# Kernel optimization log

Hardware: AMD Instinct MI355X
Metric: run time of the kernel (lower is better)

The kernel has to match this reference:

```python
import jax, jax.numpy as jnp
import numpy as np

B, T, C, H = 1, 4096, 512, 8
HS = C // H  # head size = 64
ROPE_BASE = 10000.0


def setup_inputs() -> dict:
    key = jax.random.key(0)
    k1, k2, k3 = jax.random.split(key, 3)
    x = jax.random.normal(k1, (B, T, C), dtype=jnp.float32)
    W_attn = jax.random.normal(k2, (3 * C, C), dtype=jnp.float32) * 0.02
    W_proj = jax.random.normal(k3, (C, C), dtype=jnp.float32) * 0.02
    # RoPE cache: (T, HS//2, 2) = (cos, sin) per position/frequency
    pos = jnp.arange(T, dtype=jnp.float32)
    inv_freq = 1.0 / (ROPE_BASE ** (jnp.arange(0, HS, 2, dtype=jnp.float32) / HS))
    ang = pos[:, None] * inv_freq[None, :]  # (T, HS//2)
    rope = jnp.stack([jnp.cos(ang), jnp.sin(ang)], axis=-1)
    # causal mask (1,1,T,T), True = attend
    mask = jnp.tril(jnp.ones((T, T), dtype=bool))[None, None]
    return {"x": x, "rope": rope, "mask": mask, "W_attn": W_attn, "W_proj": W_proj}


def apply_rope(x, rope):
    # x: (B, T, H, hs); rope: (>=T, hs//2, 2)
    b, t, h, d = x.shape
    xs = x.reshape(b, t, h, d // 2, 2)
    rc = rope[:t].reshape(1, t, 1, d // 2, 2)
    real = xs[..., 0] * rc[..., 0] - xs[..., 1] * rc[..., 1]
    imag = xs[..., 1] * rc[..., 0] + xs[..., 0] * rc[..., 1]
    return jnp.stack([real, imag], axis=-1).reshape(b, t, h, d)


def reference(x, rope, mask, W_attn, W_proj):
    b, t, c = x.shape
    qkv = x @ W_attn.T  # (B,T,3C)
    q, k, v = jnp.split(qkv, 3, axis=2)
    q = q.reshape(b, t, H, HS)
    k = k.reshape(b, t, H, HS)
    v = v.reshape(b, t, H, HS)
    q = apply_rope(q, rope)
    k = apply_rope(k, rope)
    # (B,H,T,hs)
    q = q.transpose(0, 2, 1, 3)
    k = k.transpose(0, 2, 1, 3)
    v = v.transpose(0, 2, 1, 3)
    scores = jnp.einsum('bhqd,bhkd->bhqk', q, k) * (1.0 / np.sqrt(HS).astype(np.float32))
    scores = jnp.where(mask, scores, -jnp.inf)
    att = jax.nn.softmax(scores, axis=-1)
    y = jnp.einsum('bhqk,bhkd->bhqd', att, v)
    y = y.transpose(0, 2, 1, 3).reshape(b, t, c)
    return y @ W_proj.T
```

## Files before the change

### kernel.cpp

```cpp
#include <hip/hip_runtime.h>

#define T_ 4096
#define C_ 512
#define H_ 8
#define HS_ 64

typedef __attribute__((ext_vector_type(8))) short s16x8;
typedef __attribute__((ext_vector_type(4))) float f32x4;
typedef unsigned int u32;

__device__ __forceinline__ float bf2f(short u) {
    union { float f; unsigned int i; } v;
    v.i = ((unsigned int)(unsigned short)u) << 16;
    return v.f;
}
__device__ __forceinline__ short f2bf(float f) {
    union { float f; unsigned int i; } v;
    v.f = f;
    unsigned int r = (v.i + 0x7FFFu + ((v.i >> 16) & 1u)) >> 16;
    return (short)r;
}

__device__ __forceinline__ void gload_lds16(const short* g, short* l) {
    __builtin_amdgcn_global_load_lds((const __attribute__((address_space(1))) u32*)g,
                                     (__attribute__((address_space(3))) u32*)l,
                                     16, 0, 0);
}

__global__ void cvt3_kernel(const float* __restrict__ x, const float* __restrict__ wa,
                            const float* __restrict__ wp,
                            short* __restrict__ xb, short* __restrict__ wab,
                            short* __restrict__ wpb) {
    int b = blockIdx.x, tid = threadIdx.x;
    const float* src; short* dst; int i;
    if (b < 2048)      { src = x;  dst = xb;  i = b * 256 + tid; }
    else if (b < 2816) { src = wa; dst = wab; i = (b - 2048) * 256 + tid; }
    else               { src = wp; dst = wpb; i = (b - 2816) * 256 + tid; }
    float4 v = ((const float4*)src)[i];
    short4 o;
    o.x = f2bf(v.x); o.y = f2bf(v.y); o.z = f2bf(v.z); o.w = f2bf(v.w);
    ((short4*)dst)[i] = o;
}

template <int BM, int BN, int OUT_BF16>
__global__ __launch_bounds__(256) void gemm_bt(const short* __restrict__ A,
                                               const short* __restrict__ B,
                                               void* __restrict__ Cv,
                                               int M, int N, int K) {
    __shared__ __align__(16) short As[BM][64];
    __shared__ __align__(16) short Bs[BN][64];
    constexpr int WM = BM / 2, WN = BN / 2;
    constexpr int MR = WM / 16, NR = WN / 16;
    int bn = blockIdx.x, bm = blockIdx.y;
    int tid = threadIdx.x;
    int lane = tid & 63, w = tid >> 6;
    int wr = w >> 1, wc = w & 1;
    int lr = lane & 15, lg = lane >> 4;

    f32x4 acc[MR][NR];
#pragma unroll
    for (int m = 0; m < MR; ++m)
#pragma unroll
        for (int n = 0; n < NR; ++n) acc[m][n] = f32x4{0.f, 0.f, 0.f, 0.f};

    const short* Ab = A + (size_t)bm * BM * K;
    const short* Bb = B + (size_t)bn * BN * K;

    for (int k0 = 0; k0 < K; k0 += 64) {
#pragma unroll
        for (int i = 0; i < BM / 32; ++i) {
            int c = i * 256 + tid;
            int row = c >> 3, cb = (c & 7) ^ (row & 7);
            gload_lds16(Ab + (size_t)row * K + k0 + cb * 8, &As[0][0] + c * 8);
        }
#pragma unroll
        for (int i = 0; i < BN / 32; ++i) {
            int c = i * 256 + tid;
            int row = c >> 3, cb = (c & 7) ^ (row & 7);
            gload_lds16(Bb + (size_t)row * K + k0 + cb * 8, &Bs[0][0] + c * 8);
        }
        __syncthreads();
#pragma unroll
        for (int kk = 0; kk < 2; ++kk) {
            s16x8 af[MR], bf[NR];
#pragma unroll
            for (int m = 0; m < MR; ++m) {
                int row = wr * WM + m * 16 + lr;
                af[m] = *(const s16x8*)&As[row][(((kk * 4 + lg) ^ (row & 7)) << 3)];
            }
#pragma unroll
            for (int n = 0; n < NR; ++n) {
                int row = wc * WN + n * 16 + lr;
                bf[n] = *(const s16x8*)&Bs[row][(((kk * 4 + lg) ^ (row & 7)) << 3)];
            }
#pragma unroll
            for (int m = 0; m < MR; ++m)
#pragma unroll
                for (int n = 0; n < NR; ++n)
                    acc[m][n] = __builtin_amdgcn_mfma_f32_16x16x32_bf16(af[m], bf[n], acc[m][n], 0, 0, 0);
        }
        __syncthreads();
    }

#pragma unroll
    for (int m = 0; m < MR; ++m) {
        int row = bm * BM + wr * WM + m * 16 + lg * 4;
#pragma unroll
        for (int n = 0; n < NR; ++n) {
            int col = bn * BN + wc * WN + n * 16 + lr;
#pragma unroll
            for (int i = 0; i < 4; ++i) {
                size_t idx = (size_t)(row + i) * N + col;
                if (OUT_BF16) ((short*)Cv)[idx] = f2bf(acc[m][n][i]);
                else          ((float*)Cv)[idx] = acc[m][n][i];
            }
        }
    }
}

__global__ __launch_bounds__(256) void prep_kernel(const short* __restrict__ qkv,
                                                   const float* __restrict__ rope,
                                                   short* __restrict__ q,
                                                   short* __restrict__ k,
                                                   short* __restrict__ vt) {
    __shared__ short tile[64][72];
    int bt = blockIdx.x, h = blockIdx.y;
    int tid = threadIdx.x;
    const float QS = 0.18033688011112042f;

#pragma unroll
    for (int r = 0; r < 2; ++r) {
        int idx = r * 256 + tid;
        int tt = idx >> 3, c8 = idx & 7;
        int t = bt * 64 + tt;
        const short* row = qkv + (size_t)t * (3 * C_) + h * 64 + c8 * 8;
        s16x8 qv = *(const s16x8*)row;
        s16x8 kv = *(const s16x8*)(row + C_);
        float4 rc0 = *(const float4*)(rope + t * 64 + c8 * 8);
        float4 rc1 = *(const float4*)(rope + t * 64 + c8 * 8 + 4);
        float cs[4] = {rc0.x, rc0.z, rc1.x, rc1.z};
        float sn[4] = {rc0.y, rc0.w, rc1.y, rc1.w};
        s16x8 qo, ko;
#pragma unroll
        for (int p = 0; p < 4; ++p) {
            float qe = bf2f(qv[2 * p]), qd = bf2f(qv[2 * p + 1]);
            float ke = bf2f(kv[2 * p]), kd = bf2f(kv[2 * p + 1]);
            qo[2 * p]     = f2bf((qe * cs[p] - qd * sn[p]) * QS);
            qo[2 * p + 1] = f2bf((qd * cs[p] + qe * sn[p]) * QS);
            ko[2 * p]     = f2bf(ke * cs[p] - kd * sn[p]);
            ko[2 * p + 1] = f2bf(kd * cs[p] + ke * sn[p]);
        }
        size_t o = ((size_t)h * T_ + t) * HS_ + c8 * 8;
        *(s16x8*)(q + o) = qo;
        *(s16x8*)(k + o) = ko;
    }

#pragma unroll
    for (int it = 0; it < 16; ++it) {
        int idx = it * 256 + tid;
        int dd = idx & 63, tt = idx >> 6;
        tile[tt][dd] = qkv[(size_t)(bt * 64 + tt) * (3 * C_) + 2 * C_ + h * 64 + dd];
    }
    __syncthreads();
#pragma unroll
    for (int it = 0; it < 16; ++it) {
        int idx = it * 256 + tid;
        int tt = idx & 63, dd = idx >> 6;
        vt[((size_t)h * HS_ + dd) * T_ + bt * 64 + tt] = tile[tt][dd];
    }
}

__global__ __launch_bounds__(256) void attn_kernel(const short* __restrict__ q,
                                                   const short* __restrict__ k,
                                                   const short* __restrict__ vt,
                                                   short* __restrict__ ypart,
                                                   float* __restrict__ lpart) {
    __shared__ __align__(16) short Ks[2][64][64];
    __shared__ __align__(16) short Vs[2][64][64];
    __shared__ __align__(16) short P[4][16][64];
    int bx = blockIdx.x;
    int h = bx & 7;
    int u = bx >> 3;
    int qb = 0, j = u;
    for (int qq = 31; qq >= 0; --qq) {
        int ncq = (qq + 4) >> 2;
        if (j < ncq) { qb = qq; break; }
        j -= ncq;
    }
    int ncq = (qb + 4) >> 2;
    int tiles = 2 * qb + 2;
    int bas = tiles / ncq, rr = tiles % ncq;
    int t0 = j * bas + (j < rr ? j : rr);
    int t1 = t0 + bas + (j < rr ? 1 : 0);

    int tid = threadIdx.x;
    int w = tid >> 6, lane = tid & 63;
    int lr = lane & 15, lg = lane >> 4, x7 = lane & 7;
    int qrow0 = qb * 128 + w * 32;
    const float MC = 12.0f;

    const short* qp = q + ((size_t)h * T_ + qrow0 + lr) * HS_ + lg * 8;
    s16x8 aq0 = *(const s16x8*)qp;
    s16x8 aq1 = *(const s16x8*)(qp + 32);
    s16x8 aq2 = *(const s16x8*)(qp + 16 * HS_);
    s16x8 aq3 = *(const s16x8*)(qp + 16 * HS_ + 32);

    s16x8 bones;
#pragma unroll
    for (int jj = 0; jj < 8; ++jj) bones[jj] = (short)0x3F80;

    f32x4 yA[4], yB[4];
#pragma unroll
    for (int n = 0; n < 4; ++n) { yA[n] = f32x4{0.f,0.f,0.f,0.f}; yB[n] = f32x4{0.f,0.f,0.f,0.f}; }
    f32x4 lAa = f32x4{0.f,0.f,0.f,0.f}, lBa = f32x4{0.f,0.f,0.f,0.f};

    const short* kH = k + (size_t)h * T_ * HS_;
    const short* vH = vt + (size_t)h * HS_ * T_;

    auto stage = [&](short* Kb, short* Vb, int t) {
#pragma unroll
        for (int r = 0; r < 2; ++r) {
            int c = r * 256 + tid;
            int row = c >> 3;
            int cb = (c & 7) ^ (row & 7);
            gload_lds16(kH + (size_t)(t * 64 + row) * HS_ + cb * 8, Kb + c * 8);
            gload_lds16(vH + (size_t)row * T_ + t * 64 + cb * 8, Vb + c * 8);
        }
    };

    short* Pw = &P[w][0][0];

    auto body = [&](int t, const short* Kb, const short* Vb) {
        f32x4 sA[4], sB[4];
#pragma unroll
        for (int c4 = 0; c4 < 4; ++c4) {
            int krow = c4 * 16 + lr;
            const short* kp = Kb + krow * 64;
            s16x8 k0 = *(const s16x8*)(kp + ((lg ^ x7) << 3));
            s16x8 k1 = *(const s16x8*)(kp + (((lg + 4) ^ x7) << 3));
            f32x4 s = f32x4{0.f,0.f,0.f,0.f};
            s = __builtin_amdgcn_mfma_f32_16x16x32_bf16(aq0, k0, s, 0, 0, 0);
            sA[c4] = __builtin_amdgcn_mfma_f32_16x16x32_bf16(aq1, k1, s, 0, 0, 0);
            f32x4 s2 = f32x4{0.f,0.f,0.f,0.f};
            s2 = __builtin_amdgcn_mfma_f32_16x16x32_bf16(aq2, k0, s2, 0, 0, 0);
            sB[c4] = __builtin_amdgcn_mfma_f32_16x16x32_bf16(aq3, k1, s2, 0, 0, 0);
        }
        if (t * 64 + 63 > qrow0) {
#pragma unroll
            for (int c4 = 0; c4 < 4; ++c4) {
                int kcol = t * 64 + c4 * 16 + lr;
#pragma unroll
                for (int i = 0; i < 4; ++i)
                    if (kcol > qrow0 + lg * 4 + i) sA[c4][i] = -1e30f;
            }
        }
        if (t * 64 + 63 > qrow0 + 16) {
#pragma unroll
            for (int c4 = 0; c4 < 4; ++c4) {
                int kcol = t * 64 + c4 * 16 + lr;
#pragma unroll
                for (int i = 0; i < 4; ++i)
                    if (kcol > qrow0 + 16 + lg * 4 + i) sB[c4][i] = -1e30f;
            }
        }
        s16x8 vf[8];
#pragma unroll
        for (int n = 0; n < 4; ++n) {
            int vrow = n * 16 + lr;
            const short* vrp = Vb + vrow * 64;
            vf[2 * n]     = *(const s16x8*)(vrp + ((lg ^ (vrow & 7)) << 3));
            vf[2 * n + 1] = *(const s16x8*)(vrp + (((lg + 4) ^ (vrow & 7)) << 3));
        }
#pragma unroll
        for (int c4 = 0; c4 < 4; ++c4)
#pragma unroll
            for (int i = 0; i < 4; ++i) {
                int row = lg * 4 + i;
                int off = row * 64 + (((c4 * 2 + (lr >> 3)) ^ (row & 7)) << 3) + (lr & 7);
                Pw[off] = f2bf(exp2f(sA[c4][i] - MC));
            }
        s16x8 ap0 = *(const s16x8*)&Pw[lr * 64 + ((lg ^ x7) << 3)];
        s16x8 ap1 = *(const s16x8*)&Pw[lr * 64 + (((lg + 4) ^ x7) << 3)];
        lAa = __builtin_amdgcn_mfma_f32_16x16x32_bf16(ap0, bones, lAa, 0, 0, 0);
        lAa = __builtin_amdgcn_mfma_f32_16x16x32_bf16(ap1, bones, lAa, 0, 0, 0);
#pragma unroll
        for (int n = 0; n < 4; ++n) {
            yA[n] = __builtin_amdgcn_mfma_f32_16x16x32_bf16(ap0, vf[2 * n], yA[n], 0, 0, 0);
            yA[n] = __builtin_amdgcn_mfma_f32_16x16x32_bf16(ap1, vf[2 * n + 1], yA[n], 0, 0, 0);
        }
#pragma unroll
        for (int c4 = 0; c4 < 4; ++c4)
#pragma unroll
            for (int i = 0; i < 4; ++i) {
                int row = lg * 4 + i;
                int off = row * 64 + (((c4 * 2 + (lr >> 3)) ^ (row & 7)) << 3) + (lr & 7);
                Pw[off] = f2bf(exp2f(sB[c4][i] - MC));
            }
        s16x8 bp0 = *(const s16x8*)&Pw[lr * 64 + ((lg ^ x7) << 3)];
        s16x8 bp1 = *(const s16x8*)&Pw[lr * 64 + (((lg + 4) ^ x7) << 3)];
        lBa = __builtin_amdgcn_mfma_f32_16x16x32_bf16(bp0, bones, lBa, 0, 0, 0);
        lBa = __builtin_amdgcn_mfma_f32_16x16x32_bf16(bp1, bones, lBa, 0, 0, 0);
#pragma unroll
        for (int n = 0; n < 4; ++n) {
            yB[n] = __builtin_amdgcn_mfma_f32_16x16x32_bf16(bp0, vf[2 * n], yB[n], 0, 0, 0);
            yB[n] = __builtin_amdgcn_mfma_f32_16x16x32_bf16(bp1, vf[2 * n + 1], yB[n], 0, 0, 0);
        }
    };

    stage(&Ks[0][0][0], &Vs[0][0][0], t0);
    __syncthreads();
    int t = t0;
    for (;;) {
        bool m1 = (t + 1 < t1);
        if (m1) stage(&Ks[1][0][0], &Vs[1][0][0], t + 1);
        body(t, &Ks[0][0][0], &Vs[0][0][0]);
        __syncthreads();
        ++t;
        if (!m1) break;
        bool m2 = (t + 1 < t1);
        if (m2) stage(&Ks[0][0][0], &Vs[0][0][0], t + 1);
        body(t, &Ks[1][0][0], &Vs[1][0][0]);
        __syncthreads();
        ++t;
        if (!m2) break;
    }

    short* yp = ypart + (((size_t)j * H_ + h) * T_ + qrow0) * HS_;
#pragma unroll
    for (int n = 0; n < 4; ++n)
#pragma unroll
        for (int i = 0; i < 4; ++i) {
            yp[(size_t)(lg * 4 + i) * HS_ + n * 16 + lr]      = f2bf(yA[n][i]);
            yp[(size_t)(16 + lg * 4 + i) * HS_ + n * 16 + lr] = f2bf(yB[n][i]);
        }
    if (lr == 0) {
#pragma unroll
        for (int i = 0; i < 4; ++i) {
            size_t r = ((size_t)j * H_ + h) * T_ + qrow0;
            lpart[r + lg * 4 + i]      = lAa[i];
            lpart[r + 16 + lg * 4 + i] = lBa[i];
        }
    }
}

__global__ void combine_kernel(const short* __restrict__ ypart,
                               const float* __restrict__ lpart,
                               short* __restrict__ y) {
    int g = blockIdx.x * 256 + threadIdx.x;
    int c8 = (g & 7) * 8;
    int row = (g >> 3) & 4095;
    int h = g >> 15;
    int nc = ((row >> 7) + 4) >> 2;
    float L = 0.f;
    float acc[8] = {0.f, 0.f, 0.f, 0.f, 0.f, 0.f, 0.f, 0.f};
    for (int c = 0; c < nc; ++c) {
        size_t base = ((size_t)c * H_ + h) * T_ + row;
        L += lpart[base];
        s16x8 yv = *(const s16x8*)(ypart + base * HS_ + c8);
#pragma unroll
        for (int jj = 0; jj < 8; ++jj) acc[jj] += bf2f(yv[jj]);
    }
    float inv = 1.f / L;
    s16x8 o;
#pragma unroll
    for (int jj = 0; jj < 8; ++jj) o[jj] = f2bf(acc[jj] * inv);
    *(s16x8*)(y + (size_t)row * C_ + h * 64 + c8) = o;
}

extern "C" void kernel_launch(void* const* d_in, const int* in_sizes, int n_in,
                              void* d_out, int out_size, void* d_ws, size_t ws_size,
                              hipStream_t stream) {
    const float* x    = (const float*)d_in[0];
    const float* rope = (const float*)d_in[1];
    const float* Wa   = (const float*)d_in[3];
    const float* Wp   = (const float*)d_in[4];
    float* out = (float*)d_out;

    short* ws   = (short*)d_ws;
    short* xb   = ws;
    short* wab  = xb + 2097152;
    short* wpb  = wab + 786432;
    short* qkvb = wpb + 262144;
    short* qws  = qkvb + 6291456;
    short* kws  = qws + 2097152;
    short* vtws = kws + 2097152;
    short* yws  = vtws + 2097152;
    short* ypart = yws + 2097152;
    float* lpart = (float*)(ypart + 16777216);

    cvt3_kernel<<<3072, 256, 0, stream>>>(x, Wa, Wp, xb, wab, wpb);

    gemm_bt<128, 128, 1><<<dim3(12, 32), 256, 0, stream>>>(xb, wab, qkvb, 4096, 1536, 512);

    prep_kernel<<<dim3(64, 8), 256, 0, stream>>>(qkvb, rope, qws, kws, vtws);

    attn_kernel<<<1152, 256, 0, stream>>>(qws, kws, vtws, ypart, lpart);
    combine_kernel<<<1024, 256, 0, stream>>>(ypart, lpart, yws);

    gemm_bt<128, 64, 0><<<dim3(8, 32), 256, 0, stream>>>(yws, wpb, out, 4096, 512, 512);
}
```

Before: 195.2 us.

## Double-buffer GEMM LDS tiles, vectorize V transpose, shrink GEMM tiles for more blocks

The GEMM now double-buffers its LDS tiles, issuing the async global-to-LDS loads for the next K slice before computing on the current one, so each iteration needs one barrier instead of two. The V transpose in the prep kernel now uses 16-byte vector loads and stores in place of scalar element copies. Both GEMM launches use smaller tiles (128x64 and 64x64), giving more blocks to fill the CUs. The cost is twice the LDS per block, and it is unclear whether overlap happens, since global_load_lds completion is tracked by vmcnt and the barrier may wait for it anyway.

```diff
diff --git a/kernel.cpp b/kernel.cpp
--- a/kernel.cpp
+++ b/kernel.cpp
@@ -47,8 +47,8 @@
                                                const short* __restrict__ B,
                                                void* __restrict__ Cv,
                                                int M, int N, int K) {
-    __shared__ __align__(16) short As[BM][64];
-    __shared__ __align__(16) short Bs[BN][64];
+    __shared__ __align__(16) short As[2][BM][64];
+    __shared__ __align__(16) short Bs[2][BN][64];
     constexpr int WM = BM / 2, WN = BN / 2;
     constexpr int MR = WM / 16, NR = WN / 16;
     int bn = blockIdx.x, bm = blockIdx.y;
@@ -66,32 +66,33 @@
     const short* Ab = A + (size_t)bm * BM * K;
     const short* Bb = B + (size_t)bn * BN * K;
 
-    for (int k0 = 0; k0 < K; k0 += 64) {
+    auto stage = [&](int k0, int b) {
 #pragma unroll
         for (int i = 0; i < BM / 32; ++i) {
             int c = i * 256 + tid;
             int row = c >> 3, cb = (c & 7) ^ (row & 7);
-            gload_lds16(Ab + (size_t)row * K + k0 + cb * 8, &As[0][0] + c * 8);
+            gload_lds16(Ab + (size_t)row * K + k0 + cb * 8, &As[b][0][0] + c * 8);
         }
 #pragma unroll
         for (int i = 0; i < BN / 32; ++i) {
             int c = i * 256 + tid;
             int row = c >> 3, cb = (c & 7) ^ (row & 7);
-            gload_lds16(Bb + (size_t)row * K + k0 + cb * 8, &Bs[0][0] + c * 8);
-        }
-        __syncthreads();
+            gload_lds16(Bb + (size_t)row * K + k0 + cb * 8, &Bs[b][0][0] + c * 8);
+        }
+    };
+    auto compute = [&](int b) {
 #pragma unroll
         for (int kk = 0; kk < 2; ++kk) {
             s16x8 af[MR], bf[NR];
 #pragma unroll
             for (int m = 0; m < MR; ++m) {
                 int row = wr * WM + m * 16 + lr;
-                af[m] = *(const s16x8*)&As[row][(((kk * 4 + lg) ^ (row & 7)) << 3)];
+                af[m] = *(const s16x8*)&As[b][row][(((kk * 4 + lg) ^ (row & 7)) << 3)];
             }
 #pragma unroll
             for (int n = 0; n < NR; ++n) {
                 int row = wc * WN + n * 16 + lr;
-                bf[n] = *(const s16x8*)&Bs[row][(((kk * 4 + lg) ^ (row & 7)) << 3)];
+                bf[n] = *(const s16x8*)&Bs[b][row][(((kk * 4 + lg) ^ (row & 7)) << 3)];
             }
 #pragma unroll
             for (int m = 0; m < MR; ++m)
@@ -99,6 +100,15 @@
                 for (int n = 0; n < NR; ++n)
                     acc[m][n] = __builtin_amdgcn_mfma_f32_16x16x32_bf16(af[m], bf[n], acc[m][n], 0, 0, 0);
         }
+    };
+
+    stage(0, 0);
+    __syncthreads();
+    int nt = K / 64;
+    for (int t = 0; t < nt; ++t) {
+        int b = t & 1;
+        if (t + 1 < nt) stage((t + 1) * 64, b ^ 1);
+        compute(b);
         __syncthreads();
     }
 
@@ -156,17 +166,21 @@
     }
 
 #pragma unroll
-    for (int it = 0; it < 16; ++it) {
-        int idx = it * 256 + tid;
-        int dd = idx & 63, tt = idx >> 6;
-        tile[tt][dd] = qkv[(size_t)(bt * 64 + tt) * (3 * C_) + 2 * C_ + h * 64 + dd];
+    for (int r = 0; r < 2; ++r) {
+        int idx = r * 256 + tid;
+        int tt = idx >> 3, c8 = idx & 7;
+        *(s16x8*)&tile[tt][c8 * 8] =
+            *(const s16x8*)(qkv + (size_t)(bt * 64 + tt) * (3 * C_) + 2 * C_ + h * 64 + c8 * 8);
     }
     __syncthreads();
 #pragma unroll
-    for (int it = 0; it < 16; ++it) {
-        int idx = it * 256 + tid;
-        int tt = idx & 63, dd = idx >> 6;
-        vt[((size_t)h * HS_ + dd) * T_ + bt * 64 + tt] = tile[tt][dd];
+    for (int r = 0; r < 2; ++r) {
+        int idx = r * 256 + tid;
+        int dd = idx & 63, tg = idx >> 6;
+        s16x8 o;
+#pragma unroll
+        for (int j = 0; j < 8; ++j) o[j] = tile[tg * 8 + j][dd];
+        *(s16x8*)(vt + ((size_t)h * HS_ + dd) * T_ + bt * 64 + tg * 8) = o;
     }
 }
 
@@ -390,12 +404,12 @@
 
     cvt3_kernel<<<3072, 256, 0, stream>>>(x, Wa, Wp, xb, wab, wpb);
 
-    gemm_bt<128, 128, 1><<<dim3(12, 32), 256, 0, stream>>>(xb, wab, qkvb, 4096, 1536, 512);
+    gemm_bt<128, 64, 1><<<dim3(24, 32), 256, 0, stream>>>(xb, wab, qkvb, 4096, 1536, 512);
 
     prep_kernel<<<dim3(64, 8), 256, 0, stream>>>(qkvb, rope, qws, kws, vtws);
 
     attn_kernel<<<1152, 256, 0, stream>>>(qws, kws, vtws, ypart, lpart);
     combine_kernel<<<1024, 256, 0, stream>>>(ypart, lpart, yws);
 
-    gemm_bt<128, 64, 0><<<dim3(8, 32), 256, 0, stream>>>(yws, wpb, out, 4096, 512, 512);
-}
+    gemm_bt<64, 64, 0><<<dim3(8, 64), 256, 0, stream>>>(yws, wpb, out, 4096, 512, 512);
+}
```

Result: faster. 181.4 us (-7.1%).
